# Performance work log

Hardware: AMD Instinct MI355X
Metric: run time of the kernel (lower is better)

## Reference

```python
import jax, jax.numpy as jnp
import numpy as np

B, S, HID = 2, 2048, 4096
NH, NKV, HD = 32, 8, 128
GROUPS = NH // NKV
THETA = 10000.0
SUPPRESS = 0.1


def setup_inputs() -> dict:
    key = jax.random.key(0)
    ks = jax.random.split(key, 8)
    hidden_states = jax.random.normal(ks[0], (B, S, HID), jnp.float32)
    sc = 0.02
    Wq = jax.random.normal(ks[1], (NH * HD, HID), jnp.float32) * sc
    Wk = jax.random.normal(ks[2], (NKV * HD, HID), jnp.float32) * sc
    Wv = jax.random.normal(ks[3], (NKV * HD, HID), jnp.float32) * sc
    Wo = jax.random.normal(ks[4], (HID, NH * HD), jnp.float32) * sc
    # additive causal mask [B,1,S,S]
    causal = jnp.where(jnp.tril(jnp.ones((S, S), bool)), 0.0, jnp.finfo(jnp.float32).min)
    attention_mask = jnp.broadcast_to(causal[None, None], (B, 1, S, S)).astype(jnp.float32)
    position_ids = jnp.broadcast_to(jnp.arange(S, dtype=jnp.int32)[None], (B, S))
    tgt_pos = jax.random.randint(ks[5], (B,), S // 2, S, dtype=jnp.int32)
    subject_positions = jax.random.randint(ks[6], (B, 8), 0, S // 2, dtype=jnp.int32)
    return dict(hidden_states=hidden_states, Wq=Wq, Wk=Wk, Wv=Wv, Wo=Wo,
                attention_mask=attention_mask, position_ids=position_ids,
                tgt_pos=tgt_pos, subject_positions=subject_positions)


def _rope_cos_sin(position_ids):
    inv_freq = 1.0 / (THETA ** (jnp.arange(0, HD, 2, dtype=jnp.float32) / HD))  # [HD/2]
    freqs = position_ids.astype(jnp.float32)[:, :, None] * inv_freq[None, None, :]  # [B,S,HD/2]
    emb = jnp.concatenate([freqs, freqs], axis=-1)  # [B,S,HD]
    return jnp.cos(emb), jnp.sin(emb)


def _rotate_half(x):
    x1, x2 = jnp.split(x, 2, axis=-1)
    return jnp.concatenate([-x2, x1], axis=-1)


def reference(hidden_states, Wq, Wk, Wv, Wo, attention_mask, position_ids, tgt_pos, subject_positions):
    b, s, _ = hidden_states.shape
    q = (hidden_states @ Wq.T).reshape(b, s, NH, HD).transpose(0, 2, 1, 3)   # [B,NH,S,HD]
    k = (hidden_states @ Wk.T).reshape(b, s, NKV, HD).transpose(0, 2, 1, 3)  # [B,NKV,S,HD]
    v = (hidden_states @ Wv.T).reshape(b, s, NKV, HD).transpose(0, 2, 1, 3)

    cos, sin = _rope_cos_sin(position_ids)  # [B,S,HD]
    cos, sin = cos[:, None], sin[:, None]   # broadcast over heads
    q = q * cos + _rotate_half(q) * sin
    k = k * cos + _rotate_half(k) * sin

    # repeat_kv for GQA
    k = jnp.repeat(k, GROUPS, axis=1)  # [B,NH,S,HD]
    v = jnp.repeat(v, GROUPS, axis=1)

    attn = jnp.einsum('bhqd,bhkd->bhqk', q, k) / jnp.sqrt(jnp.float32(HD))
    attn = attn + attention_mask
    attn = jax.nn.softmax(attn.astype(jnp.float32), axis=-1).astype(q.dtype)

    # per-token suppression: attn[b,:,tgt_pos[b],subject_positions[b,:]] *= c
    b_idx = jnp.arange(b)
    attn = attn.at[b_idx[:, None], :, tgt_pos[:, None], subject_positions].multiply(SUPPRESS)

    out = jnp.einsum('bhqk,bhkd->bhqd', attn, v)        # [B,NH,S,HD]
    out = out.transpose(0, 2, 1, 3).reshape(b, s, NH * HD)
    return out @ Wo.T
```

## Files before the change

### kernel.cpp

```cpp
#include <hip/hip_runtime.h>
#include <math.h>

typedef float f32x4 __attribute__((ext_vector_type(4)));
typedef unsigned int u32x4 __attribute__((ext_vector_type(4)));
typedef unsigned short u16x4 __attribute__((ext_vector_type(4)));
typedef __bf16 bf16x8 __attribute__((ext_vector_type(8)));

#define SCALE_Q 0.08838834764831845f
#define SCALE_Q_LOG2E 0.1275174270f

__device__ __forceinline__ float bf2f(unsigned short u) {
  unsigned int x = ((unsigned int)u) << 16;
  return __builtin_bit_cast(float, x);
}
__device__ __forceinline__ unsigned short f2bf(float f) {
  unsigned int u = __builtin_bit_cast(unsigned int, f);
  u += 0x7fffu + ((u >> 16) & 1u);
  return (unsigned short)(u >> 16);
}
__device__ __forceinline__ float fexp2(float x) {
  float r;
  asm("v_exp_f32 %0, %1" : "=v"(r) : "v"(x));
  return r;
}
__device__ __forceinline__ unsigned int cvtpk_bf16(float lo, float hi) {
  unsigned int r;
  asm("v_cvt_pk_bf16_f32 %0, %1, %2" : "=v"(r) : "v"(lo), "v"(hi));
  return r;
}

__device__ __forceinline__ void gload_lds16(const unsigned short* g, unsigned short* l) {
  __builtin_amdgcn_global_load_lds((const __attribute__((address_space(1))) unsigned int*)g,
                                   (__attribute__((address_space(3))) unsigned int*)l,
                                   16, 0, 0);
}

__global__ __launch_bounds__(256) void cvt_all(const float* __restrict__ h,
                                               const float* __restrict__ wq,
                                               const float* __restrict__ wk,
                                               const float* __restrict__ wv,
                                               const float* __restrict__ wo,
                                               unsigned short* __restrict__ Xb,
                                               unsigned short* __restrict__ Wqkvb,
                                               unsigned short* __restrict__ Wob) {
  int i = blockIdx.x * 256 + threadIdx.x;
  const float* src;
  unsigned short* dst;
  int off;
  if (i < 4194304)        { src = h;  dst = Xb;                off = i; }
  else if (i < 8388608)   { src = wq; dst = Wqkvb;             off = i - 4194304; }
  else if (i < 9437184)   { src = wk; dst = Wqkvb + 16777216;  off = i - 8388608; }
  else if (i < 10485760)  { src = wv; dst = Wqkvb + 20971520;  off = i - 9437184; }
  else                    { src = wo; dst = Wob;               off = i - 10485760; }
  f32x4 v = *(const f32x4*)(src + (size_t)off * 4);
  u16x4 o;
  o[0] = f2bf(v[0]); o[1] = f2bf(v[1]); o[2] = f2bf(v[2]); o[3] = f2bf(v[3]);
  *(u16x4*)(dst + (size_t)off * 4) = o;
}

template <int BF16OUT>
__global__ __launch_bounds__(512, 2) void gemm256(const unsigned short* __restrict__ A,
                                                  const unsigned short* __restrict__ B,
                                                  float* __restrict__ Cf,
                                                  unsigned short* __restrict__ Cb,
                                                  int M, int N, int K) {
  extern __shared__ __align__(16) unsigned short lds[];
  const int tid = threadIdx.x, lane = tid & 63, wv = tid >> 6;
  const int l16 = lane & 15, g16 = lane >> 4;
  const int m0 = blockIdx.y * 256, n0 = blockIdx.x * 256;
  const int wm = (wv >> 2) * 128, wn = (wv & 3) * 64;

  const unsigned short* aptr[4];
  const unsigned short* bptr[4];
  int adst[4], bdst[4];
#pragma unroll
  for (int j = 0; j < 4; ++j) {
    int S = (wv < 4) ? (4 * j + wv) : (16 + 4 * j + (wv - 4));
    int row = (S >> 1) * 16 + (lane >> 2);
    int col = (S & 1) * 32 + (((lane & 3) * 8) ^ ((lane >> 5) << 4));
    aptr[j] = A + (size_t)(m0 + row) * K + col;
    bptr[j] = B + (size_t)(n0 + row) * K + col;
    adst[j] = S * 512;
    bdst[j] = 16384 + S * 512;
  }

#define SLOT(j, bufoff, koff)                              \
  do {                                                     \
    gload_lds16(aptr[j] + (koff), lds + (bufoff) + adst[j]); \
    gload_lds16(bptr[j] + (koff), lds + (bufoff) + bdst[j]); \
  } while (0)

  f32x4 acc[8][4] = {};
  const int NT = K >> 6;

  SLOT(0, 0, 0); SLOT(1, 0, 0); SLOT(2, 0, 0); SLOT(3, 0, 0);
  SLOT(0, 32768, 64); SLOT(1, 32768, 64); SLOT(2, 32768, 64);
  asm volatile("s_waitcnt vmcnt(6)" ::: "memory");
  __builtin_amdgcn_s_barrier();

  const int rdo = l16 * 32 + ((g16 * 8) ^ ((l16 >> 3) << 4));

  for (int t = 0; t < NT; ++t) {
    const int p = t & 1;
    const unsigned short* La = lds + p * 32768;
    const unsigned short* Lb = La + 16384;
    const int cur = p * 32768, oth = 32768 - cur;
    const int kn1 = ((t + 1 < NT) ? t + 1 : NT - 1) * 64;
    const int kn2 = ((t + 2 < NT) ? t + 2 : NT - 1) * 64;

    bf16x8 bfr[4][2];

    {
#pragma unroll
      for (int ni = 0; ni < 4; ++ni) {
        int sb = ((wn + ni * 16) >> 4) * 2;
#pragma unroll
        for (int ks = 0; ks < 2; ++ks)
          bfr[ni][ks] = *(const bf16x8*)&Lb[(sb + ks) * 512 + rdo];
      }
      bf16x8 afr[2][2];
#pragma unroll
      for (int j = 0; j < 2; ++j) {
        int sb = ((wm + j * 16) >> 4) * 2;
#pragma unroll
        for (int ks = 0; ks < 2; ++ks)
          afr[j][ks] = *(const bf16x8*)&La[(sb + ks) * 512 + rdo];
      }
      SLOT(3, oth, kn1);
      __builtin_amdgcn_s_barrier();
      asm volatile("s_waitcnt lgkmcnt(0)" ::: "memory");
      __builtin_amdgcn_sched_barrier(0);
      __builtin_amdgcn_s_setprio(1);
#pragma unroll
      for (int j = 0; j < 2; ++j)
#pragma unroll
        for (int ni = 0; ni < 4; ++ni)
#pragma unroll
          for (int ks = 0; ks < 2; ++ks)
            acc[j][ni] = __builtin_amdgcn_mfma_f32_16x16x32_bf16(
                afr[j][ks], bfr[ni][ks], acc[j][ni], 0, 0, 0);
      __builtin_amdgcn_s_setprio(0);
      __builtin_amdgcn_s_barrier();
    }

#pragma unroll
    for (int q = 1; q < 4; ++q) {
      bf16x8 afr[2][2];
#pragma unroll
      for (int j = 0; j < 2; ++j) {
        int sb = ((wm + (q * 2 + j) * 16) >> 4) * 2;
#pragma unroll
        for (int ks = 0; ks < 2; ++ks)
          afr[j][ks] = *(const bf16x8*)&La[(sb + ks) * 512 + rdo];
      }
      if (q == 1) SLOT(0, cur, kn2);
      if (q == 2) SLOT(1, cur, kn2);
      if (q == 3) {
        SLOT(2, cur, kn2);
        asm volatile("s_waitcnt vmcnt(6)" ::: "memory");
      }
      __builtin_amdgcn_s_barrier();
      asm volatile("s_waitcnt lgkmcnt(0)" ::: "memory");
      __builtin_amdgcn_sched_barrier(0);
      __builtin_amdgcn_s_setprio(1);
#pragma unroll
      for (int j = 0; j < 2; ++j)
#pragma unroll
        for (int ni = 0; ni < 4; ++ni)
#pragma unroll
          for (int ks = 0; ks < 2; ++ks)
            acc[q * 2 + j][ni] = __builtin_amdgcn_mfma_f32_16x16x32_bf16(
                afr[j][ks], bfr[ni][ks], acc[q * 2 + j][ni], 0, 0, 0);
      __builtin_amdgcn_s_setprio(0);
      __builtin_amdgcn_s_barrier();
    }
  }
  asm volatile("s_waitcnt vmcnt(0)" ::: "memory");
#undef SLOT

#pragma unroll
  for (int mi = 0; mi < 8; ++mi)
#pragma unroll
    for (int ni = 0; ni < 4; ++ni) {
      int row = m0 + wm + mi * 16 + g16 * 4;
      int col = n0 + wn + ni * 16 + l16;
#pragma unroll
      for (int r = 0; r < 4; ++r) {
        if (BF16OUT) Cb[(size_t)(row + r) * N + col] = f2bf(acc[mi][ni][r]);
        else         Cf[(size_t)(row + r) * N + col] = acc[mi][ni][r];
      }
    }
}

__global__ __launch_bounds__(256) void rope_vtrans(const unsigned short* __restrict__ C1,
                                                   const int* __restrict__ pos_ids,
                                                   unsigned short* __restrict__ Qb,
                                                   unsigned short* __restrict__ Kb,
                                                   unsigned short* __restrict__ Vt) {
  __shared__ __align__(16) unsigned short T[64 * 72];
  const int bid = blockIdx.x;
  if (bid < 40960) {
    int idx = bid * 256 + threadIdx.x;
    int i = idx & 63;
    int t = idx >> 6;
    int head = t % 40;
    int m = t / 40;
    int b = m >> 11, s = m & 2047;
    const unsigned short* src = C1 + (size_t)m * 6144 + head * 128;
    float x1 = bf2f(src[i]), x2 = bf2f(src[i + 64]);
    float invf = exp2f((float)i * -0.2076205059304601f);
    float ang = (float)pos_ids[m] * invf;
    float c, sn;
    sincosf(ang, &sn, &c);
    float o1 = x1 * c - x2 * sn;
    float o2 = x2 * c + x1 * sn;
    unsigned short* dst;
    float scl = 1.0f;
    if (head < 32) {
      dst = Qb + ((size_t)(b * 32 + head) * 2048 + s) * 128;
      scl = SCALE_Q_LOG2E;
    } else {
      dst = Kb + ((size_t)(b * 8 + head - 32) * 2048 + s) * 128;
    }
    dst[i] = f2bf(o1 * scl);
    dst[i + 64] = f2bf(o2 * scl);
  } else {
    const int v = bid - 40960;
    const int s0 = (v & 31) * 64;
    const int d0 = ((v >> 5) & 1) * 64;
    const int bh = v >> 6;
    const int t = threadIdx.x;
    {
      int sl = t >> 2, c16 = (t & 3) * 16;
      const unsigned short* src =
          C1 + (size_t)((bh >> 3) * 2048 + s0 + sl) * 6144 + 5120 + (bh & 7) * 128 + d0 + c16;
      u32x4 a0 = *(const u32x4*)src;
      u32x4 a1 = *(const u32x4*)(src + 8);
      *(u32x4*)&T[sl * 72 + c16] = a0;
      *(u32x4*)&T[sl * 72 + c16 + 8] = a1;
    }
    __syncthreads();
    {
      int dl = t >> 2, s16 = (t & 3) * 16;
      unsigned short* dst = Vt + ((size_t)bh * 128 + d0 + dl) * 2048 + s0 + s16;
      u16x4 o[4];
#pragma unroll
      for (int j = 0; j < 16; ++j) ((unsigned short*)o)[j] = T[(s16 + j) * 72 + dl];
#pragma unroll
      for (int q = 0; q < 4; ++q) *(u16x4*)(dst + q * 4) = o[q];
    }
  }
}

__global__ __launch_bounds__(512, 4) void flash_fwd(const unsigned short* __restrict__ Q,
                                                    const unsigned short* __restrict__ K,
                                                    const unsigned short* __restrict__ Vt,
                                                    const int* __restrict__ tgt,
                                                    const int* __restrict__ subj,
                                                    unsigned short* __restrict__ AO) {
  __shared__ __align__(16) unsigned short Ks[64 * 128];
  __shared__ __align__(16) unsigned short VT[128 * 64];
  __shared__ __align__(16) unsigned short Pl[128 * 72];

  const int id = blockIdx.x;
  const int xs = id & 7;
  const int kk = id >> 3;
  const int s = xs + 8 * (kk >> 5);
  const int bis = kk & 31;
  const int b = s >> 3, kvh = s & 7;
  const int h = kvh * 4 + (bis >> 3);
  const int qpair = bis & 7;

  const int tid = threadIdx.x, lane = tid & 63, wv = tid >> 6;
  const int l16 = lane & 15, g16 = lane >> 4;
  const unsigned short* Qp = Q + (size_t)(b * 32 + h) * 2048 * 128;
  const unsigned short* Kp = K + (size_t)(b * 8 + kvh) * 2048 * 128;
  const unsigned short* Vp = Vt + (size_t)(b * 8 + kvh) * 128 * 2048;

  const int trow = tgt[b];
  int sj[8];
#pragma unroll
  for (int i2 = 0; i2 < 8; ++i2) sj[i2] = subj[b * 8 + i2];

  bf16x8 onesf;
#pragma unroll
  for (int j = 0; j < 8; ++j) onesf[j] = (__bf16)1.0f;

  const int st_row = tid >> 4;
  const int st_cb = (tid & 15) * 16;
  const int vd = tid >> 2;
  const int vq = (tid & 3) * 32;

  char* ksdst[2];
  char* vtdst[2];
#pragma unroll
  for (int p = 0; p < 2; ++p)
    ksdst[p] = (char*)Ks + (p * 32 + st_row) * 256 + (st_cb ^ ((st_row & 7) << 4));
#pragma unroll
  for (int e = 0; e < 2; ++e)
    vtdst[e] = (char*)VT + vd * 128 + ((vq + e * 16) ^ ((vd & 7) << 4));

  for (int pass = 0; pass < 2; ++pass) {
    const int qt = pass == 0 ? (15 - qpair) : qpair;
    const int nkb = 2 * qt + 2;

    bf16x8 qf[4];
    {
      int qrow = qt * 128 + wv * 16 + l16;
#pragma unroll
      for (int ks = 0; ks < 4; ++ks)
        qf[ks] = *(const bf16x8*)&Qp[(size_t)qrow * 128 + ks * 32 + g16 * 8];
    }

    float m_r[4] = {-1e30f, -1e30f, -1e30f, -1e30f};
    f32x4 lacc = {0.f, 0.f, 0.f, 0.f};
    float ldelta = 0.f;
    f32x4 ao[8] = {};

    const bool supp_tile = (trow >> 7) == qt;
    const bool supp_me = supp_tile && (((trow & 127) >> 4) == wv) && (((trow & 15) >> 2) == g16);
    const int supp_r = trow & 3;

    u32x4 kreg[2], vreg[2];
#pragma unroll
    for (int p = 0; p < 2; ++p)
      kreg[p] = *(const u32x4*)&Kp[(size_t)(p * 32 + st_row) * 128 + (st_cb >> 1)];
#pragma unroll
    for (int e = 0; e < 2; ++e)
      vreg[e] = *(const u32x4*)&Vp[(size_t)vd * 2048 + (vq >> 1) + e * 8];

    for (int kb = 0; kb < nkb; ++kb) {
      __syncthreads();
#pragma unroll
      for (int p = 0; p < 2; ++p) *(u32x4*)ksdst[p] = kreg[p];
#pragma unroll
      for (int e = 0; e < 2; ++e) *(u32x4*)vtdst[e] = vreg[e];
      if (kb + 1 < nkb) {
#pragma unroll
        for (int p = 0; p < 2; ++p)
          kreg[p] = *(const u32x4*)&Kp[(size_t)((kb + 1) * 64 + p * 32 + st_row) * 128 +
                                       (st_cb >> 1)];
#pragma unroll
        for (int e = 0; e < 2; ++e)
          vreg[e] = *(const u32x4*)&Vp[(size_t)vd * 2048 + (kb + 1) * 64 + (vq >> 1) + e * 8];
      }
      __syncthreads();

      f32x4 sc[4] = {};
      __builtin_amdgcn_s_setprio(1);
#pragma unroll
      for (int kt = 0; kt < 4; ++kt) {
#pragma unroll
        for (int ks = 0; ks < 4; ++ks) {
          int row = kt * 16 + l16;
          int cb = ks * 64 + g16 * 16;
          bf16x8 kf = *(const bf16x8*)((const char*)Ks + row * 256 + (cb ^ ((row & 7) << 4)));
          sc[kt] = __builtin_amdgcn_mfma_f32_16x16x32_bf16(qf[ks], kf, sc[kt], 0, 0, 0);
        }
      }
      __builtin_amdgcn_s_setprio(0);

      int qrow0 = qt * 128 + wv * 16 + g16 * 4;
      float p_[4][4];
      if (kb >= 2 * qt) {
#pragma unroll
        for (int kt = 0; kt < 4; ++kt)
#pragma unroll
          for (int r = 0; r < 4; ++r) {
            int kc = kb * 64 + kt * 16 + l16;
            p_[kt][r] = (kc <= qrow0 + r) ? sc[kt][r] : -INFINITY;
          }
      } else {
#pragma unroll
        for (int kt = 0; kt < 4; ++kt)
#pragma unroll
          for (int r = 0; r < 4; ++r) p_[kt][r] = sc[kt][r];
      }

      float lmx[4];
#pragma unroll
      for (int r = 0; r < 4; ++r)
        lmx[r] = fmaxf(fmaxf(p_[0][r], p_[1][r]), fmaxf(p_[2][r], p_[3][r]));
      bool need = (lmx[0] > m_r[0] + 11.0f) || (lmx[1] > m_r[1] + 11.0f) ||
                  (lmx[2] > m_r[2] + 11.0f) || (lmx[3] > m_r[3] + 11.0f);
      if (__any(need ? 1 : 0)) {
        float rescv[4];
#pragma unroll
        for (int r = 0; r < 4; ++r) {
          float mx = lmx[r];
#pragma unroll
          for (int off = 8; off; off >>= 1) mx = fmaxf(mx, __shfl_xor(mx, off));
          float mnew = fmaxf(m_r[r], mx);
          bool keep = (mnew - m_r[r]) <= 11.0f;
          rescv[r] = keep ? 1.0f : fexp2(m_r[r] - mnew);
          m_r[r] = keep ? m_r[r] : mnew;
        }
#pragma unroll
        for (int dt = 0; dt < 8; ++dt)
#pragma unroll
          for (int r = 0; r < 4; ++r) ao[dt][r] *= rescv[r];
#pragma unroll
        for (int r = 0; r < 4; ++r) lacc[r] *= rescv[r];
        ldelta *= rescv[supp_r];
      }
#pragma unroll
      for (int kt = 0; kt < 4; ++kt)
#pragma unroll
        for (int r = 0; r < 4; ++r) p_[kt][r] = fexp2(p_[kt][r] - m_r[r]);

      if (supp_me) {
#pragma unroll
        for (int kt = 0; kt < 4; ++kt) {
          int kc = kb * 64 + kt * 16 + l16;
          float f = 1.f;
#pragma unroll
          for (int i2 = 0; i2 < 8; ++i2)
            if (sj[i2] == kc) f *= 0.1f;
#pragma unroll
          for (int r = 0; r < 4; ++r)
            if (r == supp_r) {
              float before = p_[kt][r];
              p_[kt][r] = before * f;
              ldelta += before - p_[kt][r];
            }
        }
      }

      {
        int qb0 = (wv * 16 + g16 * 4) * 72 + l16;
#pragma unroll
        for (int kt = 0; kt < 4; ++kt) {
          unsigned int p01 = cvtpk_bf16(p_[kt][0], p_[kt][1]);
          unsigned int p23 = cvtpk_bf16(p_[kt][2], p_[kt][3]);
          int col = kt * 16;
          Pl[qb0 + col]           = (unsigned short)p01;
          Pl[qb0 + 72 + col]      = (unsigned short)(p01 >> 16);
          Pl[qb0 + 144 + col]     = (unsigned short)p23;
          Pl[qb0 + 216 + col]     = (unsigned short)(p23 >> 16);
        }
      }

      bf16x8 pa[2];
#pragma unroll
      for (int kc = 0; kc < 2; ++kc)
        pa[kc] = *(const bf16x8*)&Pl[(wv * 16 + l16) * 72 + kc * 32 + g16 * 8];

      __builtin_amdgcn_s_setprio(1);
#pragma unroll
      for (int kc = 0; kc < 2; ++kc)
        lacc = __builtin_amdgcn_mfma_f32_16x16x32_bf16(pa[kc], onesf, lacc, 0, 0, 0);
#pragma unroll
      for (int dt = 0; dt < 8; ++dt) {
#pragma unroll
        for (int kc = 0; kc < 2; ++kc) {
          bf16x8 vf = *(const bf16x8*)((const char*)VT + (dt * 16 + l16) * 128 +
                                       ((kc * 64 + g16 * 16) ^ ((l16 & 7) << 4)));
          ao[dt] = __builtin_amdgcn_mfma_f32_16x16x32_bf16(pa[kc], vf, ao[dt], 0, 0, 0);
        }
      }
      __builtin_amdgcn_s_setprio(0);
    }

#pragma unroll
    for (int off = 8; off; off >>= 1) ldelta += __shfl_xor(ldelta, off);

    int qrow = qt * 128 + wv * 16 + g16 * 4;
#pragma unroll
    for (int r = 0; r < 4; ++r) {
      float lfin = lacc[r] + ((r == supp_r) ? ldelta : 0.f);
      float inv = 1.0f / lfin;
#pragma unroll
      for (int dt = 0; dt < 8; ++dt)
        AO[((size_t)b * 2048 + qrow + r) * 4096 + h * 128 + dt * 16 + l16] =
            f2bf(ao[dt][r] * inv);
    }
  }
}

extern "C" void kernel_launch(void* const* d_in, const int* in_sizes, int n_in,
                              void* d_out, int out_size, void* d_ws, size_t ws_size,
                              hipStream_t stream) {
  const float* hidden = (const float*)d_in[0];
  const float* Wq = (const float*)d_in[1];
  const float* Wk = (const float*)d_in[2];
  const float* Wv = (const float*)d_in[3];
  const float* Wo = (const float*)d_in[4];
  const int* pos = (const int*)d_in[6];
  const int* tgt = (const int*)d_in[7];
  const int* subj = (const int*)d_in[8];
  float* out = (float*)d_out;

  unsigned short* ws = (unsigned short*)d_ws;
  unsigned short* Xb    = ws;
  unsigned short* Wqkvb = Xb + (size_t)16777216;
  unsigned short* Wob   = Wqkvb + (size_t)25165824;
  unsigned short* C1    = Wob + (size_t)16777216;
  unsigned short* Qb    = C1 + (size_t)25165824;
  unsigned short* Kb    = Qb + (size_t)16777216;
  unsigned short* Vt    = Kb + (size_t)4194304;
  unsigned short* AO    = Vt + (size_t)4194304;

  (void)hipFuncSetAttribute(reinterpret_cast<const void*>(gemm256<1>),
                            hipFuncAttributeMaxDynamicSharedMemorySize, 131072);
  (void)hipFuncSetAttribute(reinterpret_cast<const void*>(gemm256<0>),
                            hipFuncAttributeMaxDynamicSharedMemorySize, 131072);

  cvt_all<<<57344, 256, 0, stream>>>(hidden, Wq, Wk, Wv, Wo, Xb, Wqkvb, Wob);

  gemm256<1><<<dim3(24, 16), 512, 131072, stream>>>(Xb, Wqkvb, nullptr, C1, 4096, 6144, 4096);

  rope_vtrans<<<41984, 256, 0, stream>>>(C1, pos, Qb, Kb, Vt);

  flash_fwd<<<512, 512, 0, stream>>>(Qb, Kb, Vt, tgt, subj, AO);

  gemm256<0><<<dim3(16, 16), 512, 131072, stream>>>(AO, Wob, out, nullptr, 4096, 4096, 4096);
}
```

Before: 533.0 us.

## Rewrite flash attention with 32x32 MFMA, S^T layout and register-resident P

The attention kernel moves from 16x16x32 to 32x32x16 bf16 MFMAs, computing S transposed so each lane owns one query row. Softmax statistics therefore need no cross-lane shuffles, and P is repacked into the A operand with lane shuffles instead of going through a shared-memory buffer. Blocks shrink to 256 threads (4 waves of 32 query rows), and each thread now loads more K/V per stage. The intent is to cut LDS traffic and reduction overhead and get better MFMA efficiency, at the cost of more registers per thread and fewer waves per block.

Result: slower. 581.5 us (+9.1%).

```diff
diff --git a/kernel.cpp b/kernel.cpp
--- a/kernel.cpp
+++ b/kernel.cpp
@@ -2,6 +2,7 @@
 #include <math.h>
 
 typedef float f32x4 __attribute__((ext_vector_type(4)));
+typedef float f32x16 __attribute__((ext_vector_type(16)));
 typedef unsigned int u32x4 __attribute__((ext_vector_type(4)));
 typedef unsigned short u16x4 __attribute__((ext_vector_type(4)));
 typedef __bf16 bf16x8 __attribute__((ext_vector_type(8)));
@@ -252,7 +253,7 @@
   }
 }
 
-__global__ __launch_bounds__(512, 4) void flash_fwd(const unsigned short* __restrict__ Q,
+__global__ __launch_bounds__(256, 2) void flash_fwd(const unsigned short* __restrict__ Q,
                                                     const unsigned short* __restrict__ K,
                                                     const unsigned short* __restrict__ Vt,
                                                     const int* __restrict__ tgt,
@@ -260,7 +261,7 @@
                                                     unsigned short* __restrict__ AO) {
   __shared__ __align__(16) unsigned short Ks[64 * 128];
   __shared__ __align__(16) unsigned short VT[128 * 64];
-  __shared__ __align__(16) unsigned short Pl[128 * 72];
+  __shared__ float scr[4][32];
 
   const int id = blockIdx.x;
   const int xs = id & 7;
@@ -271,8 +272,8 @@
   const int h = kvh * 4 + (bis >> 3);
   const int qpair = bis & 7;
 
-  const int tid = threadIdx.x, lane = tid & 63, wv = tid >> 6;
-  const int l16 = lane & 15, g16 = lane >> 4;
+  const int tid = threadIdx.x, lane = tid & 63, wq = tid >> 6;
+  const int q31 = lane & 31, hi = lane >> 5;
   const unsigned short* Qp = Q + (size_t)(b * 32 + h) * 2048 * 128;
   const unsigned short* Kp = K + (size_t)(b * 8 + kvh) * 2048 * 128;
   const unsigned short* Vp = Vt + (size_t)(b * 8 + kvh) * 128 * 2048;
@@ -288,192 +289,190 @@
 
   const int st_row = tid >> 4;
   const int st_cb = (tid & 15) * 16;
-  const int vd = tid >> 2;
-  const int vq = (tid & 3) * 32;
-
-  char* ksdst[2];
-  char* vtdst[2];
-#pragma unroll
-  for (int p = 0; p < 2; ++p)
-    ksdst[p] = (char*)Ks + (p * 32 + st_row) * 256 + (st_cb ^ ((st_row & 7) << 4));
-#pragma unroll
-  for (int e = 0; e < 2; ++e)
-    vtdst[e] = (char*)VT + vd * 128 + ((vq + e * 16) ^ ((vd & 7) << 4));
+  const int vd = tid >> 1;
+  const int vh = tid & 1;
+  char* ksdst[4];
+  char* vtdst[4];
+#pragma unroll
+  for (int p = 0; p < 4; ++p)
+    ksdst[p] = (char*)Ks + (p * 16 + st_row) * 256 + (st_cb ^ ((st_row & 7) << 4));
+#pragma unroll
+  for (int j = 0; j < 4; ++j)
+    vtdst[j] = (char*)VT + vd * 128 + ((vh * 64 + j * 16) ^ ((vd & 7) << 4));
 
   for (int pass = 0; pass < 2; ++pass) {
     const int qt = pass == 0 ? (15 - qpair) : qpair;
     const int nkb = 2 * qt + 2;
-
-    bf16x8 qf[4];
-    {
-      int qrow = qt * 128 + wv * 16 + l16;
-#pragma unroll
-      for (int ks = 0; ks < 4; ++ks)
-        qf[ks] = *(const bf16x8*)&Qp[(size_t)qrow * 128 + ks * 32 + g16 * 8];
-    }
-
-    float m_r[4] = {-1e30f, -1e30f, -1e30f, -1e30f};
-    f32x4 lacc = {0.f, 0.f, 0.f, 0.f};
+    const int qrow = qt * 128 + wq * 32 + q31;
+
+    bf16x8 qf[8];
+#pragma unroll
+    for (int sd = 0; sd < 8; ++sd)
+      qf[sd] = *(const bf16x8*)&Qp[(size_t)qrow * 128 + sd * 16 + hi * 8];
+
+    float m_r = -1e30f;
+    f32x16 lacc = {};
+    f32x16 ao[4] = {};
     float ldelta = 0.f;
-    f32x4 ao[8] = {};
 
     const bool supp_tile = (trow >> 7) == qt;
-    const bool supp_me = supp_tile && (((trow & 127) >> 4) == wv) && (((trow & 15) >> 2) == g16);
-    const int supp_r = trow & 3;
-
-    u32x4 kreg[2], vreg[2];
-#pragma unroll
-    for (int p = 0; p < 2; ++p)
-      kreg[p] = *(const u32x4*)&Kp[(size_t)(p * 32 + st_row) * 128 + (st_cb >> 1)];
-#pragma unroll
-    for (int e = 0; e < 2; ++e)
-      vreg[e] = *(const u32x4*)&Vp[(size_t)vd * 2048 + (vq >> 1) + e * 8];
+    const bool supp_wave = supp_tile && (((trow & 127) >> 5) == wq);
+    const bool supp_lane = supp_wave && (q31 == (trow & 31));
+
+    u32x4 kreg[4], vreg[4];
+#pragma unroll
+    for (int p = 0; p < 4; ++p)
+      kreg[p] = *(const u32x4*)&Kp[(size_t)(p * 16 + st_row) * 128 + (st_cb >> 1)];
+#pragma unroll
+    for (int j = 0; j < 4; ++j)
+      vreg[j] = *(const u32x4*)&Vp[(size_t)vd * 2048 + vh * 32 + j * 8];
 
     for (int kb = 0; kb < nkb; ++kb) {
       __syncthreads();
 #pragma unroll
-      for (int p = 0; p < 2; ++p) *(u32x4*)ksdst[p] = kreg[p];
-#pragma unroll
-      for (int e = 0; e < 2; ++e) *(u32x4*)vtdst[e] = vreg[e];
+      for (int p = 0; p < 4; ++p) *(u32x4*)ksdst[p] = kreg[p];
+#pragma unroll
+      for (int j = 0; j < 4; ++j) *(u32x4*)vtdst[j] = vreg[j];
       if (kb + 1 < nkb) {
 #pragma unroll
-        for (int p = 0; p < 2; ++p)
-          kreg[p] = *(const u32x4*)&Kp[(size_t)((kb + 1) * 64 + p * 32 + st_row) * 128 +
+        for (int p = 0; p < 4; ++p)
+          kreg[p] = *(const u32x4*)&Kp[(size_t)((kb + 1) * 64 + p * 16 + st_row) * 128 +
                                        (st_cb >> 1)];
 #pragma unroll
-        for (int e = 0; e < 2; ++e)
-          vreg[e] = *(const u32x4*)&Vp[(size_t)vd * 2048 + (kb + 1) * 64 + (vq >> 1) + e * 8];
+        for (int j = 0; j < 4; ++j)
+          vreg[j] = *(const u32x4*)&Vp[(size_t)vd * 2048 + (kb + 1) * 64 + vh * 32 + j * 8];
       }
       __syncthreads();
 
-      f32x4 sc[4] = {};
+      f32x16 sc[2] = {};
       __builtin_amdgcn_s_setprio(1);
 #pragma unroll
-      for (int kt = 0; kt < 4; ++kt) {
-#pragma unroll
-        for (int ks = 0; ks < 4; ++ks) {
-          int row = kt * 16 + l16;
-          int cb = ks * 64 + g16 * 16;
-          bf16x8 kf = *(const bf16x8*)((const char*)Ks + row * 256 + (cb ^ ((row & 7) << 4)));
-          sc[kt] = __builtin_amdgcn_mfma_f32_16x16x32_bf16(qf[ks], kf, sc[kt], 0, 0, 0);
+      for (int cb = 0; cb < 2; ++cb) {
+        int krow = cb * 32 + q31;
+        const char* kbase = (const char*)Ks + krow * 256;
+        int kxor = (krow & 7) << 4;
+#pragma unroll
+        for (int sd = 0; sd < 8; ++sd) {
+          bf16x8 kf = *(const bf16x8*)(kbase + ((sd * 32 + hi * 16) ^ kxor));
+          sc[cb] = __builtin_amdgcn_mfma_f32_32x32x16_bf16(kf, qf[sd], sc[cb], 0, 0, 0);
         }
       }
       __builtin_amdgcn_s_setprio(0);
 
-      int qrow0 = qt * 128 + wv * 16 + g16 * 4;
-      float p_[4][4];
       if (kb >= 2 * qt) {
 #pragma unroll
-        for (int kt = 0; kt < 4; ++kt)
-#pragma unroll
-          for (int r = 0; r < 4; ++r) {
-            int kc = kb * 64 + kt * 16 + l16;
-            p_[kt][r] = (kc <= qrow0 + r) ? sc[kt][r] : -INFINITY;
+        for (int cb = 0; cb < 2; ++cb)
+#pragma unroll
+          for (int reg = 0; reg < 16; ++reg) {
+            int kc = kb * 64 + cb * 32 + (reg & 3) + 8 * (reg >> 2) + 4 * hi;
+            if (kc > qrow) sc[cb][reg] = -INFINITY;
           }
-      } else {
-#pragma unroll
-        for (int kt = 0; kt < 4; ++kt)
-#pragma unroll
-          for (int r = 0; r < 4; ++r) p_[kt][r] = sc[kt][r];
-      }
-
-      float lmx[4];
-#pragma unroll
-      for (int r = 0; r < 4; ++r)
-        lmx[r] = fmaxf(fmaxf(p_[0][r], p_[1][r]), fmaxf(p_[2][r], p_[3][r]));
-      bool need = (lmx[0] > m_r[0] + 11.0f) || (lmx[1] > m_r[1] + 11.0f) ||
-                  (lmx[2] > m_r[2] + 11.0f) || (lmx[3] > m_r[3] + 11.0f);
-      if (__any(need ? 1 : 0)) {
-        float rescv[4];
-#pragma unroll
-        for (int r = 0; r < 4; ++r) {
-          float mx = lmx[r];
-#pragma unroll
-          for (int off = 8; off; off >>= 1) mx = fmaxf(mx, __shfl_xor(mx, off));
-          float mnew = fmaxf(m_r[r], mx);
-          bool keep = (mnew - m_r[r]) <= 11.0f;
-          rescv[r] = keep ? 1.0f : fexp2(m_r[r] - mnew);
-          m_r[r] = keep ? m_r[r] : mnew;
+      }
+
+      float lmax = -1e30f;
+#pragma unroll
+      for (int cb = 0; cb < 2; ++cb)
+#pragma unroll
+        for (int reg = 0; reg < 16; ++reg) lmax = fmaxf(lmax, sc[cb][reg]);
+      if (__any((lmax > m_r + 11.0f) ? 1 : 0)) {
+        float pmax = fmaxf(lmax, __shfl_xor(lmax, 32));
+        float mnew = fmaxf(m_r, pmax);
+        bool keep = (mnew - m_r) <= 11.0f;
+        float rescv = keep ? 1.0f : fexp2(m_r - mnew);
+        m_r = keep ? m_r : mnew;
+        ldelta *= rescv;
+        if (hi == 0) scr[wq][q31] = rescv;
+        float rv[16];
+#pragma unroll
+        for (int reg = 0; reg < 16; ++reg)
+          rv[reg] = scr[wq][(reg & 3) + 8 * (reg >> 2) + 4 * hi];
+#pragma unroll
+        for (int reg = 0; reg < 16; ++reg) {
+          lacc[reg] *= rv[reg];
+#pragma unroll
+          for (int db = 0; db < 4; ++db) ao[db][reg] *= rv[reg];
         }
-#pragma unroll
-        for (int dt = 0; dt < 8; ++dt)
-#pragma unroll
-          for (int r = 0; r < 4; ++r) ao[dt][r] *= rescv[r];
-#pragma unroll
-        for (int r = 0; r < 4; ++r) lacc[r] *= rescv[r];
-        ldelta *= rescv[supp_r];
-      }
-#pragma unroll
-      for (int kt = 0; kt < 4; ++kt)
-#pragma unroll
-        for (int r = 0; r < 4; ++r) p_[kt][r] = fexp2(p_[kt][r] - m_r[r]);
-
-      if (supp_me) {
-#pragma unroll
-        for (int kt = 0; kt < 4; ++kt) {
-          int kc = kb * 64 + kt * 16 + l16;
-          float f = 1.f;
-#pragma unroll
-          for (int i2 = 0; i2 < 8; ++i2)
-            if (sj[i2] == kc) f *= 0.1f;
-#pragma unroll
-          for (int r = 0; r < 4; ++r)
-            if (r == supp_r) {
-              float before = p_[kt][r];
-              p_[kt][r] = before * f;
-              ldelta += before - p_[kt][r];
-            }
+      }
+
+#pragma unroll
+      for (int cb = 0; cb < 2; ++cb)
+#pragma unroll
+        for (int reg = 0; reg < 16; ++reg) sc[cb][reg] = fexp2(sc[cb][reg] - m_r);
+
+      if (supp_lane) {
+#pragma unroll
+        for (int cb = 0; cb < 2; ++cb)
+#pragma unroll
+          for (int reg = 0; reg < 16; ++reg) {
+            int kc = kb * 64 + cb * 32 + (reg & 3) + 8 * (reg >> 2) + 4 * hi;
+            float f = 1.f;
+#pragma unroll
+            for (int i2 = 0; i2 < 8; ++i2)
+              if (sj[i2] == kc) f *= 0.1f;
+            float before = sc[cb][reg];
+            sc[cb][reg] = before * f;
+            ldelta += before - sc[cb][reg];
+          }
+      }
+
+      bf16x8 pa[2][2];
+#pragma unroll
+      for (int cb = 0; cb < 2; ++cb) {
+        unsigned int w[8];
+#pragma unroll
+        for (int u = 0; u < 8; ++u) w[u] = cvtpk_bf16(sc[cb][2 * u], sc[cb][2 * u + 1]);
+        unsigned int z0 = __shfl_xor(hi ? w[0] : w[2], 32);
+        unsigned int z1 = __shfl_xor(hi ? w[1] : w[3], 32);
+        unsigned int z2 = __shfl_xor(hi ? w[4] : w[6], 32);
+        unsigned int z3 = __shfl_xor(hi ? w[5] : w[7], 32);
+        u32x4 A0, A1;
+        A0[0] = hi ? z0 : w[0];
+        A0[1] = hi ? z1 : w[1];
+        A0[2] = hi ? w[2] : z0;
+        A0[3] = hi ? w[3] : z1;
+        A1[0] = hi ? z2 : w[4];
+        A1[1] = hi ? z3 : w[5];
+        A1[2] = hi ? w[6] : z2;
+        A1[3] = hi ? w[7] : z3;
+        pa[cb][0] = __builtin_bit_cast(bf16x8, A0);
+        pa[cb][1] = __builtin_bit_cast(bf16x8, A1);
+      }
+
+      __builtin_amdgcn_s_setprio(1);
+#pragma unroll
+      for (int cb = 0; cb < 2; ++cb)
+#pragma unroll
+        for (int tt = 0; tt < 2; ++tt) {
+          lacc = __builtin_amdgcn_mfma_f32_32x32x16_bf16(pa[cb][tt], onesf, lacc, 0, 0, 0);
+#pragma unroll
+          for (int db = 0; db < 4; ++db) {
+            int vrow = db * 32 + q31;
+            bf16x8 vf = *(const bf16x8*)((const char*)VT + vrow * 128 +
+                                         ((cb * 64 + tt * 32 + hi * 16) ^ ((vrow & 7) << 4)));
+            ao[db] = __builtin_amdgcn_mfma_f32_32x32x16_bf16(pa[cb][tt], vf, ao[db], 0, 0, 0);
+          }
         }
-      }
-
-      {
-        int qb0 = (wv * 16 + g16 * 4) * 72 + l16;
-#pragma unroll
-        for (int kt = 0; kt < 4; ++kt) {
-          unsigned int p01 = cvtpk_bf16(p_[kt][0], p_[kt][1]);
-          unsigned int p23 = cvtpk_bf16(p_[kt][2], p_[kt][3]);
-          int col = kt * 16;
-          Pl[qb0 + col]           = (unsigned short)p01;
-          Pl[qb0 + 72 + col]      = (unsigned short)(p01 >> 16);
-          Pl[qb0 + 144 + col]     = (unsigned short)p23;
-          Pl[qb0 + 216 + col]     = (unsigned short)(p23 >> 16);
-        }
-      }
-
-      bf16x8 pa[2];
-#pragma unroll
-      for (int kc = 0; kc < 2; ++kc)
-        pa[kc] = *(const bf16x8*)&Pl[(wv * 16 + l16) * 72 + kc * 32 + g16 * 8];
-
-      __builtin_amdgcn_s_setprio(1);
-#pragma unroll
-      for (int kc = 0; kc < 2; ++kc)
-        lacc = __builtin_amdgcn_mfma_f32_16x16x32_bf16(pa[kc], onesf, lacc, 0, 0, 0);
-#pragma unroll
-      for (int dt = 0; dt < 8; ++dt) {
-#pragma unroll
-        for (int kc = 0; kc < 2; ++kc) {
-          bf16x8 vf = *(const bf16x8*)((const char*)VT + (dt * 16 + l16) * 128 +
-                                       ((kc * 64 + g16 * 16) ^ ((l16 & 7) << 4)));
-          ao[dt] = __builtin_amdgcn_mfma_f32_16x16x32_bf16(pa[kc], vf, ao[dt], 0, 0, 0);
-        }
-      }
       __builtin_amdgcn_s_setprio(0);
     }
 
-#pragma unroll
-    for (int off = 8; off; off >>= 1) ldelta += __shfl_xor(ldelta, off);
-
-    int qrow = qt * 128 + wv * 16 + g16 * 4;
-#pragma unroll
-    for (int r = 0; r < 4; ++r) {
-      float lfin = lacc[r] + ((r == supp_r) ? ldelta : 0.f);
-      float inv = 1.0f / lfin;
-#pragma unroll
-      for (int dt = 0; dt < 8; ++dt)
-        AO[((size_t)b * 2048 + qrow + r) * 4096 + h * 128 + dt * 16 + l16] =
-            f2bf(ao[dt][r] * inv);
-    }
+    float ld2 = ldelta + __shfl_xor(ldelta, 32);
+    float ldb = __shfl(ld2, trow & 31);
+
+    float inv[16];
+#pragma unroll
+    for (int reg = 0; reg < 16; ++reg) {
+      float lfin = lacc[reg];
+      if (supp_wave && ((reg & 3) + 8 * (reg >> 2) + 4 * hi) == (trow & 31)) lfin += ldb;
+      inv[reg] = 1.0f / lfin;
+    }
+#pragma unroll
+    for (int db = 0; db < 4; ++db)
+#pragma unroll
+      for (int reg = 0; reg < 16; ++reg) {
+        int qq = qt * 128 + wq * 32 + (reg & 3) + 8 * (reg >> 2) + 4 * hi;
+        AO[((size_t)b * 2048 + qq) * 4096 + h * 128 + db * 32 + q31] =
+            f2bf(ao[db][reg] * inv[reg]);
+      }
   }
 }
 
@@ -511,7 +510,7 @@
 
   rope_vtrans<<<41984, 256, 0, stream>>>(C1, pos, Qb, Kb, Vt);
 
-  flash_fwd<<<512, 512, 0, stream>>>(Qb, Kb, Vt, tgt, subj, AO);
+  flash_fwd<<<512, 256, 0, stream>>>(Qb, Kb, Vt, tgt, subj, AO);
 
   gemm256<0><<<dim3(16, 16), 512, 131072, stream>>>(AO, Wob, out, nullptr, 4096, 4096, 4096);
 }
```
